# Kernel tuning notes

Measured on AMD Instinct MI355X. Metric: run time of the kernel, lower is better.

The kernel has to match this reference:

```python
import jax, jax.numpy as jnp
import numpy as np

N, E, T = 20000, 320000, 64
INP, EMB, OUT = 128, 16, 3
HEADS, MSIZE, MDIM, KDIM, VDIM = 4, 1024, 128, 64, 64


def setup_inputs() -> dict:
    key = jax.random.key(0)
    ks = iter(jax.random.split(key, 64))

    def nrm(shape, s=0.05):
        return jax.random.normal(next(ks), shape, dtype=jnp.float32) * s

    return dict(
        x=jax.random.normal(next(ks), (N, INP), dtype=jnp.float32),
        edge_index=jax.random.randint(next(ks), (2, E), 0, N),
        index=5,
        inp_types=jax.random.randint(next(ks), (T,), 0, 4),
        log_return=jax.random.normal(next(ks), (T,), dtype=jnp.float32),
        # SAGEConv 1 (SoftmaxAggregation temp t1, lin_l/lin_r, bias=False)
        t1=jnp.ones((1, INP), jnp.float32),
        W1l=nrm((INP, 512)), W1r=nrm((INP, 512)),
        ln1g_w=jnp.ones((512,), jnp.float32), ln1g_b=jnp.zeros((512,), jnp.float32),
        # SAGEConv 2
        t2=jnp.ones((1, 512), jnp.float32),
        W2l=nrm((512, 256)), W2r=nrm((512, 256)),
        ln2g_w=jnp.ones((256,), jnp.float32), ln2g_b=jnp.zeros((256,), jnp.float32),
        # MemPooling(256,128,heads=4,num_clusters=1)
        mp_k=nrm((HEADS, 1, 256), 1.0),
        mp_conv=nrm((HEADS,), 0.5),            # Conv2d(heads,1,1,bias=False)
        mp_lin=nrm((256, 128)),                # Linear(in,out,bias=False)
        fxg_w=nrm((128, 256)), fxg_b=jnp.zeros((256,), jnp.float32),
        # PolicyNet head
        emb=nrm((4, EMB), 1.0),
        fk_w=nrm((256, KDIM)), fk_b=jnp.zeros((KDIM,), jnp.float32),
        fv_w=nrm((256, VDIM)), fv_b=jnp.zeros((VDIM,), jnp.float32),
        # MultiHeadMemory
        mem=nrm((HEADS, MSIZE, MDIM), 1.0),
        mfk_w=nrm((MDIM, KDIM)), mfk_b=jnp.zeros((KDIM,), jnp.float32),
        mfv_w=nrm((MDIM, VDIM)), mfv_b=jnp.zeros((VDIM,), jnp.float32),
        mfx_w=nrm((VDIM * HEADS, VDIM)), mfx_b=jnp.zeros((VDIM,), jnp.float32),
        f1_w=nrm((INP + EMB + 2 * VDIM + 1, 512)),
        n1_w=jnp.ones((512,), jnp.float32), n1_b=jnp.zeros((512,), jnp.float32),
        f2_w=nrm((512, 256)),
        n2_w=jnp.ones((256,), jnp.float32), n2_b=jnp.zeros((256,), jnp.float32),
        f3_w=nrm((256, OUT)), f3_b=jnp.zeros((OUT,), jnp.float32),
    )


def _forward(x, t1, W1l, W1r, ln1g_w, ln1g_b, t2, W2l, W2r, ln2g_w, ln2g_b,
             mp_k, mp_conv, mp_lin, fxg_w, fxg_b, emb, fk_w, fk_b, fv_w, fv_b,
             mem, mfk_w, mfk_b, mfv_w, mfv_b, mfx_w, mfx_b,
             f1_w, n1_w, n1_b, f2_w, n2_w, n2_b, f3_w, f3_b,
             log_return, edge_index, inp_types, index):
    n = x.shape[0]
    src, dst = edge_index[0], edge_index[1]

    def sage(h, t, Wl, Wr):
        hj = h[src]                                    # [E, C] gather
        gate = hj * t                                  # learned softmax temperature
        m = jax.ops.segment_max(gate, dst, num_segments=n)
        e = jnp.exp(gate - m[dst])                     # segment-stable softmax
        s = jax.ops.segment_sum(e, dst, num_segments=n)
        agg = jax.ops.segment_sum(hj * (e / s[dst]), dst, num_segments=n)
        return agg @ Wl + h @ Wr                       # SAGEConv, bias=False

    def graph_ln(h, w, b, eps=1e-5):                   # PyG LayerNorm, mode='graph'
        hc = h - jnp.mean(h)
        return hc / jnp.sqrt(jnp.mean(hc * hc) + eps) * w + b

    h = jax.nn.relu(graph_ln(sage(x, t1, W1l, W1r), ln1g_w, ln1g_b))
    h = jax.nn.relu(graph_ln(sage(h, t2, W2l, W2r), ln2g_w, ln2g_b))

    # MemPooling (single graph => B=1), tau=1: student-t kernel over sq. distances
    H, K, C = mp_k.shape
    kk = mp_k.reshape(H * K, C)
    d2 = jnp.maximum(jnp.sum(kk * kk, 1)[:, None] - 2.0 * (kk @ h.T)
                     + jnp.sum(h * h, 1)[None, :], 0.0)        # [H*K, N]
    dist = 1.0 / (1.0 + d2)
    dist = dist.reshape(H, K, n).transpose(0, 2, 1)[None]      # [1, H, N, K]
    S = dist / jnp.sum(dist, -1, keepdims=True)
    S = jax.nn.softmax(jnp.einsum('h,bhnk->bnk', mp_conv, S), axis=-1)  # [1, N, K]
    zp = jnp.einsum('bnk,nc->bkc', S, h)[:, 0, :]              # squeeze(1), K==1
    z = (zp @ mp_lin) @ fxg_w + fxg_b                          # [1, 256]

    q = jax.nn.softmax(z @ fk_w + fk_b, axis=-1)               # [1, key_dim]
    v = z @ fv_w + fv_b                                        # [1, val_dim]

    # MultiHeadMemory
    km = jax.nn.softmax(mem @ mfk_w + mfk_b, axis=-1)          # [H, M, key]
    vm = mem @ mfv_w + mfv_b                                   # [H, M, val]
    w = jax.nn.softmax(jnp.einsum('bk,hnk->bhn', q, km), axis=-1)
    mv = jnp.einsum('bhn,hnv->bhv', w, vm).reshape(q.shape[0], -1)
    m_out = mv @ mfx_w + mfx_b                                 # [1, val]

    zz = jnp.concatenate([v, m_out], axis=-1)                  # [1, 2*val]
    t_len = inp_types.shape[0]
    xi = jnp.broadcast_to(x[index][None, :], (t_len, x.shape[1]))
    zb = jnp.broadcast_to(zz, (t_len, zz.shape[1]))
    feat = jnp.concatenate([xi, emb[inp_types], log_return.reshape(-1, 1), zb], axis=-1)

    def ln(h2, w2, b2, eps=1e-5):                              # nn.LayerNorm (last dim)
        mu = jnp.mean(h2, -1, keepdims=True)
        hc = h2 - mu
        return hc / jnp.sqrt(jnp.mean(hc * hc, -1, keepdims=True) + eps) * w2 + b2

    h1 = jax.nn.relu(ln(feat @ f1_w, n1_w, n1_b))              # dropout = identity (eval)
    h2 = jax.nn.relu(ln(h1 @ f2_w, n2_w, n2_b))
    return jax.nn.softmax(h2 @ f3_w + f3_b, axis=-1)           # [T, out_dim]


def reference(x, edge_index, index, inp_types, log_return, t1, W1l, W1r, ln1g_w, ln1g_b,
              t2, W2l, W2r, ln2g_w, ln2g_b, mp_k, mp_conv, mp_lin, fxg_w, fxg_b, emb,
              fk_w, fk_b, fv_w, fv_b, mem, mfk_w, mfk_b, mfv_w, mfv_b, mfx_w, mfx_b,
              f1_w, n1_w, n1_b, f2_w, n2_w, n2_b, f3_w, f3_b):
    return _forward(x, t1, W1l, W1r, ln1g_w, ln1g_b, t2, W2l, W2r, ln2g_w, ln2g_b,
                    mp_k, mp_conv, mp_lin, fxg_w, fxg_b, emb, fk_w, fk_b, fv_w, fv_b,
                    mem, mfk_w, mfk_b, mfv_w, mfv_b, mfx_w, mfx_b,
                    f1_w, n1_w, n1_b, f2_w, n2_w, n2_b, f3_w, f3_b,
                    log_return, edge_index, inp_types, index)
```

## Files before the change

### kernel.cpp

```cpp
#include <hip/hip_runtime.h>

typedef __attribute__((ext_vector_type(8))) short bf16x8;
typedef __attribute__((ext_vector_type(8))) unsigned short ushort8_t;
typedef __attribute__((ext_vector_type(4))) float f32x4;

__device__ __forceinline__ unsigned short f2bf(float f) {
    unsigned int x = __float_as_uint(f);
    unsigned int r = x + 0x7fffu + ((x >> 16) & 1u);
    return (unsigned short)(r >> 16);
}
__device__ __forceinline__ float bf2f(unsigned short u) {
    return __uint_as_float(((unsigned int)u) << 16);
}

__global__ void count_kernel(const int* __restrict__ dst, int E, int* __restrict__ counts) {
    int i = blockIdx.x * 256 + threadIdx.x;
    if (i < E) atomicAdd(&counts[dst[i]], 1);
}

template <int CHUNK>
__global__ __launch_bounds__(1024) void scan_kernel(const int* __restrict__ cnt,
                                                    int* __restrict__ off, int n) {
    __shared__ int s[1024];
    int tid = threadIdx.x;
    int base = tid * CHUNK;
    int loc[CHUNK];
    int sum = 0;
#pragma unroll
    for (int i = 0; i < CHUNK; ++i) {
        int idx = base + i;
        int v = (idx < n) ? cnt[idx] : 0;
        sum += v;
        loc[i] = sum;
    }
    s[tid] = sum;
    __syncthreads();
    for (int d = 1; d < 1024; d <<= 1) {
        int t = (tid >= d) ? s[tid - d] : 0;
        __syncthreads();
        s[tid] += t;
        __syncthreads();
    }
    int prev = (tid > 0) ? s[tid - 1] : 0;
    if (tid == 0) off[0] = 0;
#pragma unroll
    for (int i = 0; i < CHUNK; ++i) {
        int idx = base + i;
        if (idx < n) off[idx + 1] = prev + loc[i];
    }
}

__global__ void fill_kernel(const int* __restrict__ src, const int* __restrict__ dst, int E,
                            const int* __restrict__ off, int* __restrict__ cursor,
                            int* __restrict__ srcs) {
    int i = blockIdx.x * 256 + threadIdx.x;
    if (i < E) {
        int d = dst[i];
        int p = atomicAdd(&cursor[d], 1);
        srcs[off[d] + p] = src[i];
    }
}

__global__ __launch_bounds__(256) void cast_bf16(const float* __restrict__ in,
                                                 unsigned short* __restrict__ out, size_t n) {
    size_t stride = (size_t)gridDim.x * 256 * 4;
    for (size_t i = ((size_t)blockIdx.x * 256 + threadIdx.x) * 4; i < n; i += stride) {
        float4 v = *(const float4*)(in + i);
        ushort4 o;
        o.x = f2bf(v.x); o.y = f2bf(v.y); o.z = f2bf(v.z); o.w = f2bf(v.w);
        *(ushort4*)(out + i) = o;
    }
}

__global__ __launch_bounds__(256) void agg512(const unsigned short* __restrict__ h,
                                              const float* __restrict__ t,
                                              const int* __restrict__ off,
                                              const int* __restrict__ srcs,
                                              unsigned short* __restrict__ agg, int n) {
    int wid = threadIdx.x >> 6, lane = threadIdx.x & 63;
    int node = blockIdx.x * 4 + wid;
    if (node >= n) return;
    int beg = off[node], end = off[node + 1];
    int col = lane * 8;
    float tc[8], sE[8], sW[8];
#pragma unroll
    for (int i = 0; i < 8; ++i) { tc[i] = t[col + i]; sE[i] = 0.f; sW[i] = 0.f; }
    int e = beg;
    for (; e + 2 <= end; e += 2) {
        int s0 = srcs[e], s1 = srcs[e + 1];
        ushort8_t u0 = *(const ushort8_t*)(h + (size_t)s0 * 512 + col);
        ushort8_t u1 = *(const ushort8_t*)(h + (size_t)s1 * 512 + col);
#pragma unroll
        for (int i = 0; i < 8; ++i) {
            float v = bf2f(u0[i]);
            float w = __expf(v * tc[i]);
            sE[i] += w; sW[i] += v * w;
        }
#pragma unroll
        for (int i = 0; i < 8; ++i) {
            float v = bf2f(u1[i]);
            float w = __expf(v * tc[i]);
            sE[i] += w; sW[i] += v * w;
        }
    }
    if (e < end) {
        int s0 = srcs[e];
        ushort8_t u0 = *(const ushort8_t*)(h + (size_t)s0 * 512 + col);
#pragma unroll
        for (int i = 0; i < 8; ++i) {
            float v = bf2f(u0[i]);
            float w = __expf(v * tc[i]);
            sE[i] += w; sW[i] += v * w;
        }
    }
    ushort8_t o;
#pragma unroll
    for (int i = 0; i < 8; ++i) o[i] = f2bf((end > beg) ? (sW[i] / sE[i]) : 0.f);
    *(ushort8_t*)(agg + (size_t)node * 512 + col) = o;
}

__global__ __launch_bounds__(256) void agg128(const unsigned short* __restrict__ h,
                                              const float* __restrict__ t,
                                              const int* __restrict__ off,
                                              const int* __restrict__ srcs,
                                              unsigned short* __restrict__ agg, int n) {
    int wid = threadIdx.x >> 6, lane = threadIdx.x & 63;
    int node = blockIdx.x * 4 + wid;
    if (node >= n) return;
    int beg = off[node], end = off[node + 1];
    int col = lane * 2;
    float t0 = t[col], t1 = t[col + 1];
    float e0 = 0.f, e1 = 0.f, w0 = 0.f, w1 = 0.f;
    int e = beg;
    for (; e + 4 <= end; e += 4) {
        int s0 = srcs[e], s1 = srcs[e + 1], s2 = srcs[e + 2], s3 = srcs[e + 3];
        ushort2 u0 = *(const ushort2*)(h + (size_t)s0 * 128 + col);
        ushort2 u1 = *(const ushort2*)(h + (size_t)s1 * 128 + col);
        ushort2 u2 = *(const ushort2*)(h + (size_t)s2 * 128 + col);
        ushort2 u3 = *(const ushort2*)(h + (size_t)s3 * 128 + col);
        {
            float a = bf2f(u0.x), b = bf2f(u0.y);
            float xa = __expf(a * t0), xb = __expf(b * t1);
            e0 += xa; e1 += xb; w0 += a * xa; w1 += b * xb;
        }
        {
            float a = bf2f(u1.x), b = bf2f(u1.y);
            float xa = __expf(a * t0), xb = __expf(b * t1);
            e0 += xa; e1 += xb; w0 += a * xa; w1 += b * xb;
        }
        {
            float a = bf2f(u2.x), b = bf2f(u2.y);
            float xa = __expf(a * t0), xb = __expf(b * t1);
            e0 += xa; e1 += xb; w0 += a * xa; w1 += b * xb;
        }
        {
            float a = bf2f(u3.x), b = bf2f(u3.y);
            float xa = __expf(a * t0), xb = __expf(b * t1);
            e0 += xa; e1 += xb; w0 += a * xa; w1 += b * xb;
        }
    }
    for (; e < end; ++e) {
        int s0 = srcs[e];
        ushort2 u0 = *(const ushort2*)(h + (size_t)s0 * 128 + col);
        float a = bf2f(u0.x), b = bf2f(u0.y);
        float xa = __expf(a * t0), xb = __expf(b * t1);
        e0 += xa; e1 += xb; w0 += a * xa; w1 += b * xb;
    }
    ushort2 o;
    o.x = f2bf((end > beg) ? (w0 / e0) : 0.f);
    o.y = f2bf((end > beg) ? (w1 / e1) : 0.f);
    *(ushort2*)(agg + (size_t)node * 128 + col) = o;
}

__global__ void pack_w(const float* __restrict__ Wl, const float* __restrict__ Wr,
                       int K1, int K2, int N, unsigned short* __restrict__ Bt) {
    int idx = blockIdx.x * 256 + threadIdx.x;
    int Kc = K1 + K2;
    if (idx < N * Kc) {
        int n = idx / Kc;
        int k = idx - n * Kc;
        float v = (k < K1) ? Wl[(size_t)k * N + n] : Wr[(size_t)(k - K1) * N + n];
        Bt[idx] = f2bf(v);
    }
}

__global__ __launch_bounds__(512) void gemm_dual_mfma2(
    const unsigned short* __restrict__ A1, const unsigned short* __restrict__ A2,
    const unsigned short* __restrict__ Bt,
    unsigned short* __restrict__ Cb, double* __restrict__ part,
    int M, int N, int K1, int K2) {
    const int Kc = K1 + K2;
    __shared__ unsigned short As[128 * 40];
    __shared__ unsigned short Bs[256 * 40];
    __shared__ double rs[512], rs2[512];
    int tid = threadIdx.x;
    int lane = tid & 63, w = tid >> 6;
    int wm = w & 1, wn = w >> 1;
    int m0 = blockIdx.y * 128, n0 = blockIdx.x * 256;
    f32x4 acc[4][4] = {};
    int kg = lane >> 4, lr = lane & 15;

    for (int k0 = 0; k0 < Kc; k0 += 32) {
        const unsigned short* Asrc;
        int kk, Ksrc;
        if (k0 < K1) { Asrc = A1; kk = k0; Ksrc = K1; }
        else         { Asrc = A2; kk = k0 - K1; Ksrc = K2; }
        {
            int r = tid >> 2, ch = tid & 3;
            int gr = m0 + r;
            ushort8_t v = {0, 0, 0, 0, 0, 0, 0, 0};
            if (gr < M) v = *(const ushort8_t*)(Asrc + (size_t)gr * Ksrc + kk + ch * 8);
            *(ushort8_t*)&As[r * 40 + ch * 8] = v;
        }
#pragma unroll
        for (int it = 0; it < 2; ++it) {
            int idx = tid + it * 512;
            int r = idx >> 2, ch = idx & 3;
            const unsigned short* srcp = Bt + (size_t)(n0 + r) * Kc + k0 + ch * 8;
            *(ushort8_t*)&Bs[r * 40 + ch * 8] = *(const ushort8_t*)srcp;
        }
        __syncthreads();
        bf16x8 a[4], b[4];
#pragma unroll
        for (int i = 0; i < 4; ++i)
            a[i] = *(bf16x8*)&As[(wm * 64 + i * 16 + lr) * 40 + kg * 8];
#pragma unroll
        for (int j = 0; j < 4; ++j)
            b[j] = *(bf16x8*)&Bs[(wn * 64 + j * 16 + lr) * 40 + kg * 8];
#pragma unroll
        for (int i = 0; i < 4; ++i)
#pragma unroll
            for (int j = 0; j < 4; ++j)
                acc[i][j] = __builtin_amdgcn_mfma_f32_16x16x32_bf16(a[i], b[j], acc[i][j], 0, 0, 0);
        __syncthreads();
    }
    double s = 0, s2 = 0;
#pragma unroll
    for (int i = 0; i < 4; ++i) {
        int rbase = m0 + wm * 64 + i * 16 + kg * 4;
#pragma unroll
        for (int j = 0; j < 4; ++j) {
            int col = n0 + wn * 64 + j * 16 + lr;
#pragma unroll
            for (int reg = 0; reg < 4; ++reg) {
                int row = rbase + reg;
                if (row < M) {
                    float v = acc[i][j][reg];
                    Cb[(size_t)row * N + col] = f2bf(v);
                    s += v;
                    s2 += (double)v * v;
                }
            }
        }
    }
    rs[tid] = s;
    rs2[tid] = s2;
    __syncthreads();
    for (int d = 256; d; d >>= 1) {
        if (tid < d) { rs[tid] += rs[tid + d]; rs2[tid] += rs2[tid + d]; }
        __syncthreads();
    }
    if (tid == 0) {
        int bid = blockIdx.y * gridDim.x + blockIdx.x;
        part[bid * 2] = rs[0];
        part[bid * 2 + 1] = rs2[0];
    }
}

__global__ __launch_bounds__(256) void red_stats2d(const double* __restrict__ part, int nb,
                                                   float invn, float* __restrict__ stats) {
    __shared__ double rs[256], rs2[256];
    int tid = threadIdx.x;
    double s = 0, s2 = 0;
    for (int b = tid; b < nb; b += 256) { s += part[b * 2]; s2 += part[b * 2 + 1]; }
    rs[tid] = s; rs2[tid] = s2;
    __syncthreads();
    for (int d = 128; d; d >>= 1) {
        if (tid < d) { rs[tid] += rs[tid + d]; rs2[tid] += rs2[tid + d]; }
        __syncthreads();
    }
    if (tid == 0) {
        float mu = (float)(rs[0] * invn);
        float var = (float)(rs2[0] * invn) - mu * mu;
        stats[0] = mu;
        stats[1] = rsqrtf(var + 1e-5f);
    }
}

template <int C>
__global__ __launch_bounds__(256) void ln_relu_ip(unsigned short* __restrict__ z,
                                                  const float* __restrict__ w,
                                                  const float* __restrict__ b,
                                                  const float* __restrict__ stats, size_t n) {
    float mu = stats[0], inv = stats[1];
    size_t stride = (size_t)gridDim.x * 256 * 4;
    for (size_t i = ((size_t)blockIdx.x * 256 + threadIdx.x) * 4; i < n; i += stride) {
        ushort4 v = *(const ushort4*)(z + i);
        int c = (int)(i & (C - 1));
        ushort4 o;
        o.x = f2bf(fmaxf((bf2f(v.x) - mu) * inv * w[c] + b[c], 0.f));
        o.y = f2bf(fmaxf((bf2f(v.y) - mu) * inv * w[c + 1] + b[c + 1], 0.f));
        o.z = f2bf(fmaxf((bf2f(v.z) - mu) * inv * w[c + 2] + b[c + 2], 0.f));
        o.w = f2bf(fmaxf((bf2f(v.w) - mu) * inv * w[c + 3] + b[c + 3], 0.f));
        *(ushort4*)(z + i) = o;
    }
}

__global__ __launch_bounds__(256) void colsum_t(const unsigned short* __restrict__ h2,
                                                float* __restrict__ cspartT, int n) {
    __shared__ float red[8 * 256];
    int tid = threadIdx.x;
    int cg = tid & 31;
    int rl = tid >> 5;
    int rows_per = (n + gridDim.x - 1) / gridDim.x;
    int r0 = blockIdx.x * rows_per;
    int r1 = min(n, r0 + rows_per);
    int c8 = cg * 8;
    float acc[8] = {};
    for (int r = r0 + rl; r < r1; r += 8) {
        ushort8_t u = *(const ushort8_t*)(h2 + (size_t)r * 256 + c8);
#pragma unroll
        for (int i = 0; i < 8; ++i) acc[i] += bf2f(u[i]);
    }
#pragma unroll
    for (int i = 0; i < 8; ++i) red[rl * 256 + c8 + i] = acc[i];
    __syncthreads();
    float s = 0;
#pragma unroll
    for (int r = 0; r < 8; ++r) s += red[r * 256 + tid];
    cspartT[tid * 64 + blockIdx.x] = s;
}

__global__ __launch_bounds__(256) void zqv_kernel(const float* __restrict__ cspartT,
                                                  const float* __restrict__ mp_lin,
                                                  const float* __restrict__ fxg_w,
                                                  const float* __restrict__ fxg_b,
                                                  const float* __restrict__ fk_w,
                                                  const float* __restrict__ fk_b,
                                                  const float* __restrict__ fv_w,
                                                  const float* __restrict__ fv_b,
                                                  float* __restrict__ qv) {
    __shared__ float zp_s[256], u_s[128], z_s[256], ql_s[64];
    __shared__ float part_s[1024];
    int tid = threadIdx.x;
    {
        float s = 0;
        const float* p = cspartT + tid * 64;
#pragma unroll
        for (int i = 0; i < 16; ++i) {
            float4 v = *(const float4*)(p + i * 4);
            s += v.x + v.y + v.z + v.w;
        }
        zp_s[tid] = s;
    }
    __syncthreads();
    {
        int og = tid & 31, kc = tid >> 5;
        int j4 = og * 4;
        f32x4 a = {0.f, 0.f, 0.f, 0.f};
        for (int ci = 0; ci < 32; ++ci) {
            int c = kc * 32 + ci;
            float4 w = *(const float4*)(mp_lin + (size_t)c * 128 + j4);
            float zc = zp_s[c];
            a[0] += zc * w.x; a[1] += zc * w.y; a[2] += zc * w.z; a[3] += zc * w.w;
        }
#pragma unroll
        for (int i = 0; i < 4; ++i) part_s[kc * 128 + j4 + i] = a[i];
    }
    __syncthreads();
    if (tid < 128) {
        float s = 0;
#pragma unroll
        for (int kc = 0; kc < 8; ++kc) s += part_s[kc * 128 + tid];
        u_s[tid] = s;
    }
    __syncthreads();
    {
        int og = tid & 63, kc = tid >> 6;
        int j4 = og * 4;
        f32x4 a = {0.f, 0.f, 0.f, 0.f};
        for (int ci = 0; ci < 32; ++ci) {
            int c = kc * 32 + ci;
            float4 w = *(const float4*)(fxg_w + (size_t)c * 256 + j4);
            float uc = u_s[c];
            a[0] += uc * w.x; a[1] += uc * w.y; a[2] += uc * w.z; a[3] += uc * w.w;
        }
#pragma unroll
        for (int i = 0; i < 4; ++i) part_s[kc * 256 + j4 + i] = a[i];
    }
    __syncthreads();
    {
        float s = fxg_b[tid];
#pragma unroll
        for (int kc = 0; kc < 4; ++kc) s += part_s[kc * 256 + tid];
        z_s[tid] = s;
    }
    __syncthreads();
    {
        int og = tid & 15, kc = tid >> 4;
        int j4 = og * 4;
        f32x4 a = {0.f, 0.f, 0.f, 0.f};
        for (int ci = 0; ci < 16; ++ci) {
            int c = kc * 16 + ci;
            float4 w = *(const float4*)(fk_w + (size_t)c * 64 + j4);
            float zc = z_s[c];
            a[0] += zc * w.x; a[1] += zc * w.y; a[2] += zc * w.z; a[3] += zc * w.w;
        }
#pragma unroll
        for (int i = 0; i < 4; ++i) part_s[kc * 64 + j4 + i] = a[i];
    }
    __syncthreads();
    if (tid < 64) {
        float s = fk_b[tid];
#pragma unroll
        for (int kc = 0; kc < 16; ++kc) s += part_s[kc * 64 + tid];
        ql_s[tid] = s;
    }
    __syncthreads();
    {
        int og = tid & 15, kc = tid >> 4;
        int j4 = og * 4;
        f32x4 a = {0.f, 0.f, 0.f, 0.f};
        for (int ci = 0; ci < 16; ++ci) {
            int c = kc * 16 + ci;
            float4 w = *(const float4*)(fv_w + (size_t)c * 64 + j4);
            float zc = z_s[c];
            a[0] += zc * w.x; a[1] += zc * w.y; a[2] += zc * w.z; a[3] += zc * w.w;
        }
#pragma unroll
        for (int i = 0; i < 4; ++i) part_s[kc * 64 + j4 + i] = a[i];
    }
    __syncthreads();
    if (tid < 64) {
        float mx = ql_s[tid];
        for (int d = 32; d; d >>= 1) mx = fmaxf(mx, __shfl_xor(mx, d));
        float e = __expf(ql_s[tid] - mx);
        float s = e;
        for (int d = 32; d; d >>= 1) s += __shfl_xor(s, d);
        qv[tid] = e / s;
        float vv = fv_b[tid];
#pragma unroll
        for (int kc = 0; kc < 16; ++kc) vv += part_s[kc * 64 + tid];
        qv[64 + tid] = vv;
    }
}

__global__ __launch_bounds__(256) void mem_kv_logit(const float* __restrict__ mem,
                                                    const float* __restrict__ mfk_w,
                                                    const float* __restrict__ mfk_b,
                                                    const float* __restrict__ mfv_w,
                                                    const float* __restrict__ mfv_b,
                                                    const float* __restrict__ qv,
                                                    float* __restrict__ logits,
                                                    float* __restrict__ vm) {
    __shared__ float rows[4][128];
    __shared__ float qs[64];
    int tid = threadIdx.x;
    int r0 = blockIdx.x * 4;
    if (tid < 64) qs[tid] = qv[tid];
    for (int i = tid; i < 512; i += 256) rows[i >> 7][i & 127] = mem[(size_t)r0 * 128 + i];
    __syncthreads();
    int lr = tid >> 6;
    int lane = tid & 63;
    const float* row = rows[lr];
    float kl = mfk_b[lane], vl = mfv_b[lane];
#pragma unroll 8
    for (int c = 0; c < 128; ++c) {
        float rv = row[c];
        kl += rv * mfk_w[c * 64 + lane];
        vl += rv * mfv_w[c * 64 + lane];
    }
    float mx = kl;
    for (int d = 32; d; d >>= 1) mx = fmaxf(mx, __shfl_xor(mx, d));
    float e = __expf(kl - mx);
    float s = e;
    for (int d = 32; d; d >>= 1) s += __shfl_xor(s, d);
    float kval = e / s;
    float wl = kval * qs[lane];
    for (int d = 32; d; d >>= 1) wl += __shfl_xor(wl, d);
    size_t gr = (size_t)(r0 + lr);
    if (lane == 0) logits[gr] = wl;
    vm[gr * 64 + lane] = vl;
}

__global__ __launch_bounds__(256) void attend_part(const float* __restrict__ logits,
                                                   const float* __restrict__ vm,
                                                   float* __restrict__ part) {
    int b = blockIdx.x;
    int h = b >> 4;
    int s0 = (b & 15) * 64;
    int tid = threadIdx.x;
    __shared__ float els[64];
    __shared__ float pr[4][64];
    __shared__ float lmax_s, lsum_s;
    if (tid < 64) {
        float lg = logits[h * 1024 + s0 + tid];
        float m = lg;
        for (int d = 32; d; d >>= 1) m = fmaxf(m, __shfl_xor(m, d));
        float e = __expf(lg - m);
        els[tid] = e;
        float s = e;
        for (int d = 32; d; d >>= 1) s += __shfl_xor(s, d);
        if (tid == 0) { lmax_s = m; lsum_s = s; }
    }
    __syncthreads();
    int dd = tid & 63, g = tid >> 6;
    float acc = 0;
    for (int s = g; s < 64; s += 4)
        acc += els[s] * vm[((size_t)h * 1024 + s0 + s) * 64 + dd];
    pr[g][dd] = acc;
    __syncthreads();
    if (tid < 64) {
        float pv = pr[0][tid] + pr[1][tid] + pr[2][tid] + pr[3][tid];
        part[b * 66 + 2 + tid] = pv;
        if (tid == 0) { part[b * 66] = lmax_s; part[b * 66 + 1] = lsum_s; }
    }
}

__global__ __launch_bounds__(256) void attend_final(const float* __restrict__ part,
                                                    const float* __restrict__ mfx_w,
                                                    const float* __restrict__ mfx_b,
                                                    float* __restrict__ m_out) {
    __shared__ float mv[256];
    __shared__ float part_s[1024];
    int tid = threadIdx.x;
    int h = tid >> 6, dd = tid & 63;
    float gmax = -1e30f;
#pragma unroll
    for (int p = 0; p < 16; ++p) gmax = fmaxf(gmax, part[(h * 16 + p) * 66]);
    float total = 0.f, acc = 0.f;
#pragma unroll
    for (int p = 0; p < 16; ++p) {
        float sc = __expf(part[(h * 16 + p) * 66] - gmax);
        total += part[(h * 16 + p) * 66 + 1] * sc;
        acc += part[(h * 16 + p) * 66 + 2 + dd] * sc;
    }
    mv[h * 64 + dd] = acc / total;
    __syncthreads();
    {
        int og = tid & 15, kc = tid >> 4;
        int j4 = og * 4;
        f32x4 a = {0.f, 0.f, 0.f, 0.f};
        for (int ci = 0; ci < 16; ++ci) {
            int c = kc * 16 + ci;
            float4 w = *(const float4*)(mfx_w + (size_t)c * 64 + j4);
            float mc = mv[c];
            a[0] += mc * w.x; a[1] += mc * w.y; a[2] += mc * w.z; a[3] += mc * w.w;
        }
#pragma unroll
        for (int i = 0; i < 4; ++i) part_s[kc * 64 + j4 + i] = a[i];
    }
    __syncthreads();
    if (tid < 64) {
        float s = mfx_b[tid];
#pragma unroll
        for (int kc = 0; kc < 16; ++kc) s += part_s[kc * 64 + tid];
        m_out[tid] = s;
    }
}

__device__ __forceinline__ float block_sum_256(float v, float* red) {
    int tid = threadIdx.x;
    red[tid] = v;
    __syncthreads();
    for (int d = 128; d; d >>= 1) { if (tid < d) red[tid] += red[tid + d]; __syncthreads(); }
    float r = red[0];
    __syncthreads();
    return r;
}

__global__ __launch_bounds__(256) void head_kernel(
    const float* __restrict__ x, const int* __restrict__ index_p,
    const int* __restrict__ inp_types, const float* __restrict__ log_return,
    const float* __restrict__ emb, const float* __restrict__ qv,
    const float* __restrict__ m_out, const float* __restrict__ f1_w,
    const float* __restrict__ n1_w, const float* __restrict__ n1_b,
    const float* __restrict__ f2_w, const float* __restrict__ n2_w,
    const float* __restrict__ n2_b, const float* __restrict__ f3_w,
    const float* __restrict__ f3_b, float* __restrict__ out) {
    __shared__ float feat[273];
    __shared__ float h1[512];
    __shared__ float h2[256];
    __shared__ float red[256];
    __shared__ float l3[3];
    int r = blockIdx.x, tid = threadIdx.x;
    int idx = index_p[0];
    for (int i = tid; i < 273; i += 256) {
        float val;
        if (i < 128) val = x[(size_t)idx * 128 + i];
        else if (i < 144) val = emb[inp_types[r] * 16 + (i - 128)];
        else if (i == 144) val = log_return[r];
        else if (i < 209) val = qv[64 + (i - 145)];
        else val = m_out[i - 209];
        feat[i] = val;
    }
    __syncthreads();
    float a0 = 0, a1 = 0;
    for (int c = 0; c < 273; ++c) {
        float f = feat[c];
        a0 += f * f1_w[c * 512 + tid];
        a1 += f * f1_w[c * 512 + tid + 256];
    }
    float mu = block_sum_256(a0 + a1, red) / 512.f;
    float c0 = a0 - mu, c1 = a1 - mu;
    float var = block_sum_256(c0 * c0 + c1 * c1, red) / 512.f;
    float inv = rsqrtf(var + 1e-5f);
    h1[tid] = fmaxf(c0 * inv * n1_w[tid] + n1_b[tid], 0.f);
    h1[tid + 256] = fmaxf(c1 * inv * n1_w[tid + 256] + n1_b[tid + 256], 0.f);
    __syncthreads();
    float b0 = 0;
    for (int c = 0; c < 512; ++c) b0 += h1[c] * f2_w[c * 256 + tid];
    float mu2 = block_sum_256(b0, red) / 256.f;
    float cc = b0 - mu2;
    float var2 = block_sum_256(cc * cc, red) / 256.f;
    float inv2 = rsqrtf(var2 + 1e-5f);
    h2[tid] = fmaxf(cc * inv2 * n2_w[tid] + n2_b[tid], 0.f);
    __syncthreads();
    if (tid < 3) {
        float a = f3_b[tid];
        for (int c = 0; c < 256; ++c) a += h2[c] * f3_w[c * 3 + tid];
        l3[tid] = a;
    }
    __syncthreads();
    if (tid < 3) {
        float mx = fmaxf(l3[0], fmaxf(l3[1], l3[2]));
        float s = __expf(l3[0] - mx) + __expf(l3[1] - mx) + __expf(l3[2] - mx);
        out[r * 3 + tid] = __expf(l3[tid] - mx) / s;
    }
}

extern "C" void kernel_launch(void* const* d_in, const int* in_sizes, int n_in,
                              void* d_out, int out_size, void* d_ws, size_t ws_size,
                              hipStream_t stream) {
    const float* x = (const float*)d_in[0];
    const int* ei = (const int*)d_in[1];
    const int* index_p = (const int*)d_in[2];
    const int* inp_types = (const int*)d_in[3];
    const float* log_return = (const float*)d_in[4];
    const float* t1 = (const float*)d_in[5];
    const float* W1l = (const float*)d_in[6];
    const float* W1r = (const float*)d_in[7];
    const float* ln1g_w = (const float*)d_in[8];
    const float* ln1g_b = (const float*)d_in[9];
    const float* t2 = (const float*)d_in[10];
    const float* W2l = (const float*)d_in[11];
    const float* W2r = (const float*)d_in[12];
    const float* ln2g_w = (const float*)d_in[13];
    const float* ln2g_b = (const float*)d_in[14];
    const float* mp_lin = (const float*)d_in[17];
    const float* fxg_w = (const float*)d_in[18];
    const float* fxg_b = (const float*)d_in[19];
    const float* emb = (const float*)d_in[20];
    const float* fk_w = (const float*)d_in[21];
    const float* fk_b = (const float*)d_in[22];
    const float* fv_w = (const float*)d_in[23];
    const float* fv_b = (const float*)d_in[24];
    const float* mem = (const float*)d_in[25];
    const float* mfk_w = (const float*)d_in[26];
    const float* mfk_b = (const float*)d_in[27];
    const float* mfv_w = (const float*)d_in[28];
    const float* mfv_b = (const float*)d_in[29];
    const float* mfx_w = (const float*)d_in[30];
    const float* mfx_b = (const float*)d_in[31];
    const float* f1_w = (const float*)d_in[32];
    const float* n1_w = (const float*)d_in[33];
    const float* n1_b = (const float*)d_in[34];
    const float* f2_w = (const float*)d_in[35];
    const float* n2_w = (const float*)d_in[36];
    const float* n2_b = (const float*)d_in[37];
    const float* f3_w = (const float*)d_in[38];
    const float* f3_b = (const float*)d_in[39];
    float* out = (float*)d_out;

    int n = in_sizes[0] / 128;
    int E = in_sizes[1] / 2;
    int T = in_sizes[3];
    const int* src = ei;
    const int* dst = ei + E;

    char* w = (char*)d_ws;
    auto alloc = [&](size_t bytes) {
        char* p = w;
        w += (bytes + 255) & ~(size_t)255;
        return p;
    };
    int* counts = (int*)alloc((size_t)n * 4);
    int* off = (int*)alloc((size_t)(n + 1) * 4);
    int* srcs = (int*)alloc((size_t)E * 4);
    unsigned short* xb = (unsigned short*)alloc((size_t)n * 128 * 2);
    unsigned short* agg1b = (unsigned short*)alloc((size_t)n * 128 * 2);
    unsigned short* z1b = (unsigned short*)alloc((size_t)n * 512 * 2);
    unsigned short* agg2b = (unsigned short*)alloc((size_t)n * 512 * 2);
    unsigned short* z2b = (unsigned short*)alloc((size_t)n * 256 * 2);
    double* partd = (double*)alloc(1024 * 2 * 8);
    float* stats = (float*)alloc(2 * 4);
    float* cspartT = (float*)alloc(256 * 64 * 4);
    float* qv = (float*)alloc(128 * 4);
    float* logits = (float*)alloc((size_t)4 * 1024 * 4);
    float* vm = (float*)alloc((size_t)4 * 1024 * 64 * 4);
    float* apart = (float*)alloc(64 * 66 * 4);
    float* m_out = (float*)alloc(64 * 4);
    unsigned short* Bt1 = (unsigned short*)alloc((size_t)512 * 256 * 2);
    unsigned short* Bt2 = (unsigned short*)alloc((size_t)256 * 1024 * 2);

    int nblk_e = (E + 255) / 256;
    int mblk = (n + 127) / 128;

    hipMemsetAsync(counts, 0, (size_t)n * 4, stream);
    count_kernel<<<nblk_e, 256, 0, stream>>>(dst, E, counts);
    scan_kernel<20><<<1, 1024, 0, stream>>>(counts, off, n);
    hipMemsetAsync(counts, 0, (size_t)n * 4, stream);
    fill_kernel<<<nblk_e, 256, 0, stream>>>(src, dst, E, off, counts, srcs);

    pack_w<<<(512 * 256 + 255) / 256, 256, 0, stream>>>(W1l, W1r, 128, 128, 512, Bt1);
    pack_w<<<(256 * 1024 + 255) / 256, 256, 0, stream>>>(W2l, W2r, 512, 512, 256, Bt2);
    cast_bf16<<<1024, 256, 0, stream>>>(x, xb, (size_t)n * 128);

    agg128<<<(n + 3) / 4, 256, 0, stream>>>(xb, t1, off, srcs, agg1b, n);
    gemm_dual_mfma2<<<dim3(2, mblk), 512, 0, stream>>>(agg1b, xb, Bt1, z1b, partd, n, 512, 128, 128);
    red_stats2d<<<1, 256, 0, stream>>>(partd, 2 * mblk, 1.0f / ((float)n * 512.f), stats);
    ln_relu_ip<512><<<1024, 256, 0, stream>>>(z1b, ln1g_w, ln1g_b, stats, (size_t)n * 512);

    agg512<<<(n + 3) / 4, 256, 0, stream>>>(z1b, t2, off, srcs, agg2b, n);
    gemm_dual_mfma2<<<dim3(1, mblk), 512, 0, stream>>>(agg2b, z1b, Bt2, z2b, partd, n, 256, 512, 512);
    red_stats2d<<<1, 256, 0, stream>>>(partd, mblk, 1.0f / ((float)n * 256.f), stats);
    ln_relu_ip<256><<<512, 256, 0, stream>>>(z2b, ln2g_w, ln2g_b, stats, (size_t)n * 256);

    colsum_t<<<64, 256, 0, stream>>>(z2b, cspartT, n);
    zqv_kernel<<<1, 256, 0, stream>>>(cspartT, mp_lin, fxg_w, fxg_b, fk_w, fk_b, fv_w, fv_b, qv);

    mem_kv_logit<<<1024, 256, 0, stream>>>(mem, mfk_w, mfk_b, mfv_w, mfv_b, qv, logits, vm);
    attend_part<<<64, 256, 0, stream>>>(logits, vm, apart);
    attend_final<<<1, 256, 0, stream>>>(apart, mfx_w, mfx_b, m_out);

    head_kernel<<<T, 256, 0, stream>>>(x, index_p, inp_types, log_return, emb, qv, m_out,
                                       f1_w, n1_w, n1_b, f2_w, n2_w, n2_b, f3_w, f3_b, out);
}
```

Baseline: 292.2 us.

## Use direct global-to-LDS loads in GEMM, fuse LN stats, deepen aggregation unroll

The GEMM tile loads now use global_load_lds to copy straight into unpadded LDS, skipping the register round trip. The separate stats-reduction kernels are folded into the LayerNorm kernels, and the scan kernel zeroes the counts so one memset goes away. The aggregation loops are unrolled further, with exp2f on pre-scaled temperatures. The unpadded LDS layout may cause bank conflicts, and the A-tile load drops the row bounds check, so the last partial tile can read past M (an extra padding allocation is added).

```diff
diff --git a/kernel.cpp b/kernel.cpp
--- a/kernel.cpp
+++ b/kernel.cpp
@@ -12,6 +12,12 @@
 __device__ __forceinline__ float bf2f(unsigned short u) {
     return __uint_as_float(((unsigned int)u) << 16);
 }
+__device__ __forceinline__ void load_lds16(const void* g, void* l) {
+    __builtin_amdgcn_global_load_lds((const __attribute__((address_space(1))) void*)g,
+                                     (__attribute__((address_space(3))) void*)l, 16, 0, 0);
+}
+
+#define LOG2E 1.44269504089f
 
 __global__ void count_kernel(const int* __restrict__ dst, int E, int* __restrict__ counts) {
     int i = blockIdx.x * 256 + threadIdx.x;
@@ -19,7 +25,7 @@
 }
 
 template <int CHUNK>
-__global__ __launch_bounds__(1024) void scan_kernel(const int* __restrict__ cnt,
+__global__ __launch_bounds__(1024) void scan_kernel(int* __restrict__ cnt,
                                                     int* __restrict__ off, int n) {
     __shared__ int s[1024];
     int tid = threadIdx.x;
@@ -29,7 +35,8 @@
 #pragma unroll
     for (int i = 0; i < CHUNK; ++i) {
         int idx = base + i;
-        int v = (idx < n) ? cnt[idx] : 0;
+        int v = 0;
+        if (idx < n) { v = cnt[idx]; cnt[idx] = 0; }
         sum += v;
         loc[i] = sum;
     }
@@ -84,35 +91,28 @@
     int col = lane * 8;
     float tc[8], sE[8], sW[8];
 #pragma unroll
-    for (int i = 0; i < 8; ++i) { tc[i] = t[col + i]; sE[i] = 0.f; sW[i] = 0.f; }
+    for (int i = 0; i < 8; ++i) { tc[i] = t[col + i] * LOG2E; sE[i] = 0.f; sW[i] = 0.f; }
+#define P8(u)                                      \
+    _Pragma("unroll") for (int i = 0; i < 8; ++i) { \
+        float v = bf2f(u[i]);                       \
+        float wv = exp2f(v * tc[i]);                \
+        sE[i] += wv; sW[i] += v * wv;               \
+    }
     int e = beg;
-    for (; e + 2 <= end; e += 2) {
-        int s0 = srcs[e], s1 = srcs[e + 1];
+    for (; e + 4 <= end; e += 4) {
+        int s0 = srcs[e], s1 = srcs[e + 1], s2 = srcs[e + 2], s3 = srcs[e + 3];
         ushort8_t u0 = *(const ushort8_t*)(h + (size_t)s0 * 512 + col);
         ushort8_t u1 = *(const ushort8_t*)(h + (size_t)s1 * 512 + col);
-#pragma unroll
-        for (int i = 0; i < 8; ++i) {
-            float v = bf2f(u0[i]);
-            float w = __expf(v * tc[i]);
-            sE[i] += w; sW[i] += v * w;
-        }
-#pragma unroll
-        for (int i = 0; i < 8; ++i) {
-            float v = bf2f(u1[i]);
-            float w = __expf(v * tc[i]);
-            sE[i] += w; sW[i] += v * w;
-        }
-    }
-    if (e < end) {
+        ushort8_t u2 = *(const ushort8_t*)(h + (size_t)s2 * 512 + col);
+        ushort8_t u3 = *(const ushort8_t*)(h + (size_t)s3 * 512 + col);
+        P8(u0) P8(u1) P8(u2) P8(u3)
+    }
+    for (; e < end; ++e) {
         int s0 = srcs[e];
         ushort8_t u0 = *(const ushort8_t*)(h + (size_t)s0 * 512 + col);
-#pragma unroll
-        for (int i = 0; i < 8; ++i) {
-            float v = bf2f(u0[i]);
-            float w = __expf(v * tc[i]);
-            sE[i] += w; sW[i] += v * w;
-        }
-    }
+        P8(u0)
+    }
+#undef P8
     ushort8_t o;
 #pragma unroll
     for (int i = 0; i < 8; ++i) o[i] = f2bf((end > beg) ? (sW[i] / sE[i]) : 0.f);
@@ -129,43 +129,31 @@
     if (node >= n) return;
     int beg = off[node], end = off[node + 1];
     int col = lane * 2;
-    float t0 = t[col], t1 = t[col + 1];
+    float t0 = t[col] * LOG2E, t1 = t[col + 1] * LOG2E;
     float e0 = 0.f, e1 = 0.f, w0 = 0.f, w1 = 0.f;
+#define P2(u)                                          \
+    {                                                  \
+        float a = bf2f(u.x), b = bf2f(u.y);            \
+        float xa = exp2f(a * t0), xb = exp2f(b * t1);  \
+        e0 += xa; e1 += xb; w0 += a * xa; w1 += b * xb; \
+    }
     int e = beg;
-    for (; e + 4 <= end; e += 4) {
-        int s0 = srcs[e], s1 = srcs[e + 1], s2 = srcs[e + 2], s3 = srcs[e + 3];
-        ushort2 u0 = *(const ushort2*)(h + (size_t)s0 * 128 + col);
-        ushort2 u1 = *(const ushort2*)(h + (size_t)s1 * 128 + col);
-        ushort2 u2 = *(const ushort2*)(h + (size_t)s2 * 128 + col);
-        ushort2 u3 = *(const ushort2*)(h + (size_t)s3 * 128 + col);
-        {
-            float a = bf2f(u0.x), b = bf2f(u0.y);
-            float xa = __expf(a * t0), xb = __expf(b * t1);
-            e0 += xa; e1 += xb; w0 += a * xa; w1 += b * xb;
-        }
-        {
-            float a = bf2f(u1.x), b = bf2f(u1.y);
-            float xa = __expf(a * t0), xb = __expf(b * t1);
-            e0 += xa; e1 += xb; w0 += a * xa; w1 += b * xb;
-        }
-        {
-            float a = bf2f(u2.x), b = bf2f(u2.y);
-            float xa = __expf(a * t0), xb = __expf(b * t1);
-            e0 += xa; e1 += xb; w0 += a * xa; w1 += b * xb;
-        }
-        {
-            float a = bf2f(u3.x), b = bf2f(u3.y);
-            float xa = __expf(a * t0), xb = __expf(b * t1);
-            e0 += xa; e1 += xb; w0 += a * xa; w1 += b * xb;
-        }
+    for (; e + 8 <= end; e += 8) {
+        ushort2 u0 = *(const ushort2*)(h + (size_t)srcs[e] * 128 + col);
+        ushort2 u1 = *(const ushort2*)(h + (size_t)srcs[e + 1] * 128 + col);
+        ushort2 u2 = *(const ushort2*)(h + (size_t)srcs[e + 2] * 128 + col);
+        ushort2 u3 = *(const ushort2*)(h + (size_t)srcs[e + 3] * 128 + col);
+        ushort2 u4 = *(const ushort2*)(h + (size_t)srcs[e + 4] * 128 + col);
+        ushort2 u5 = *(const ushort2*)(h + (size_t)srcs[e + 5] * 128 + col);
+        ushort2 u6 = *(const ushort2*)(h + (size_t)srcs[e + 6] * 128 + col);
+        ushort2 u7 = *(const ushort2*)(h + (size_t)srcs[e + 7] * 128 + col);
+        P2(u0) P2(u1) P2(u2) P2(u3) P2(u4) P2(u5) P2(u6) P2(u7)
     }
     for (; e < end; ++e) {
-        int s0 = srcs[e];
-        ushort2 u0 = *(const ushort2*)(h + (size_t)s0 * 128 + col);
-        float a = bf2f(u0.x), b = bf2f(u0.y);
-        float xa = __expf(a * t0), xb = __expf(b * t1);
-        e0 += xa; e1 += xb; w0 += a * xa; w1 += b * xb;
-    }
+        ushort2 u0 = *(const ushort2*)(h + (size_t)srcs[e] * 128 + col);
+        P2(u0)
+    }
+#undef P2
     ushort2 o;
     o.x = f2bf((end > beg) ? (w0 / e0) : 0.f);
     o.y = f2bf((end > beg) ? (w1 / e1) : 0.f);
@@ -190,8 +178,8 @@
     unsigned short* __restrict__ Cb, double* __restrict__ part,
     int M, int N, int K1, int K2) {
     const int Kc = K1 + K2;
-    __shared__ unsigned short As[128 * 40];
-    __shared__ unsigned short Bs[256 * 40];
+    __shared__ unsigned short As[128 * 32];
+    __shared__ unsigned short Bs[256 * 32];
     __shared__ double rs[512], rs2[512];
     int tid = threadIdx.x;
     int lane = tid & 63, w = tid >> 6;
@@ -199,34 +187,25 @@
     int m0 = blockIdx.y * 128, n0 = blockIdx.x * 256;
     f32x4 acc[4][4] = {};
     int kg = lane >> 4, lr = lane & 15;
+    int ar = tid >> 2, ach = tid & 3;
+    int br0 = tid >> 2, bch = tid & 3;
 
     for (int k0 = 0; k0 < Kc; k0 += 32) {
         const unsigned short* Asrc;
         int kk, Ksrc;
         if (k0 < K1) { Asrc = A1; kk = k0; Ksrc = K1; }
         else         { Asrc = A2; kk = k0 - K1; Ksrc = K2; }
-        {
-            int r = tid >> 2, ch = tid & 3;
-            int gr = m0 + r;
-            ushort8_t v = {0, 0, 0, 0, 0, 0, 0, 0};
-            if (gr < M) v = *(const ushort8_t*)(Asrc + (size_t)gr * Ksrc + kk + ch * 8);
-            *(ushort8_t*)&As[r * 40 + ch * 8] = v;
-        }
-#pragma unroll
-        for (int it = 0; it < 2; ++it) {
-            int idx = tid + it * 512;
-            int r = idx >> 2, ch = idx & 3;
-            const unsigned short* srcp = Bt + (size_t)(n0 + r) * Kc + k0 + ch * 8;
-            *(ushort8_t*)&Bs[r * 40 + ch * 8] = *(const ushort8_t*)srcp;
-        }
+        load_lds16(Asrc + (size_t)(m0 + ar) * Ksrc + kk + ach * 8, &As[tid * 8]);
+        load_lds16(Bt + (size_t)(n0 + br0) * Kc + k0 + bch * 8, &Bs[tid * 8]);
+        load_lds16(Bt + (size_t)(n0 + 128 + br0) * Kc + k0 + bch * 8, &Bs[(tid + 512) * 8]);
         __syncthreads();
         bf16x8 a[4], b[4];
 #pragma unroll
         for (int i = 0; i < 4; ++i)
-            a[i] = *(bf16x8*)&As[(wm * 64 + i * 16 + lr) * 40 + kg * 8];
+            a[i] = *(bf16x8*)&As[(wm * 64 + i * 16 + lr) * 32 + kg * 8];
 #pragma unroll
         for (int j = 0; j < 4; ++j)
-            b[j] = *(bf16x8*)&Bs[(wn * 64 + j * 16 + lr) * 40 + kg * 8];
+            b[j] = *(bf16x8*)&Bs[(wn * 64 + j * 16 + lr) * 32 + kg * 8];
 #pragma unroll
         for (int i = 0; i < 4; ++i)
 #pragma unroll
@@ -267,32 +246,26 @@
     }
 }
 
-__global__ __launch_bounds__(256) void red_stats2d(const double* __restrict__ part, int nb,
-                                                   float invn, float* __restrict__ stats) {
-    __shared__ double rs[256], rs2[256];
-    int tid = threadIdx.x;
-    double s = 0, s2 = 0;
-    for (int b = tid; b < nb; b += 256) { s += part[b * 2]; s2 += part[b * 2 + 1]; }
-    rs[tid] = s; rs2[tid] = s2;
-    __syncthreads();
-    for (int d = 128; d; d >>= 1) {
-        if (tid < d) { rs[tid] += rs[tid + d]; rs2[tid] += rs2[tid + d]; }
-        __syncthreads();
-    }
-    if (tid == 0) {
-        float mu = (float)(rs[0] * invn);
-        float var = (float)(rs2[0] * invn) - mu * mu;
-        stats[0] = mu;
-        stats[1] = rsqrtf(var + 1e-5f);
-    }
-}
-
 template <int C>
 __global__ __launch_bounds__(256) void ln_relu_ip(unsigned short* __restrict__ z,
                                                   const float* __restrict__ w,
                                                   const float* __restrict__ b,
-                                                  const float* __restrict__ stats, size_t n) {
-    float mu = stats[0], inv = stats[1];
+                                                  const double* __restrict__ part, int nb,
+                                                  float invn, size_t n) {
+    __shared__ float st[2];
+    if (threadIdx.x < 64) {
+        double s = 0, s2 = 0;
+        for (int i = threadIdx.x; i < nb; i += 64) { s += part[2 * i]; s2 += part[2 * i + 1]; }
+        for (int d = 32; d; d >>= 1) { s += __shfl_down(s, d); s2 += __shfl_down(s2, d); }
+        if (threadIdx.x == 0) {
+            float mu = (float)(s * invn);
+            float var = (float)(s2 * invn) - mu * mu;
+            st[0] = mu;
+            st[1] = rsqrtf(var + 1e-5f);
+        }
+    }
+    __syncthreads();
+    float mu = st[0], inv = st[1];
     size_t stride = (size_t)gridDim.x * 256 * 4;
     for (size_t i = ((size_t)blockIdx.x * 256 + threadIdx.x) * 4; i < n; i += stride) {
         ushort4 v = *(const ushort4*)(z + i);
@@ -693,7 +666,6 @@
     unsigned short* agg2b = (unsigned short*)alloc((size_t)n * 512 * 2);
     unsigned short* z2b = (unsigned short*)alloc((size_t)n * 256 * 2);
     double* partd = (double*)alloc(1024 * 2 * 8);
-    float* stats = (float*)alloc(2 * 4);
     float* cspartT = (float*)alloc(256 * 64 * 4);
     float* qv = (float*)alloc(128 * 4);
     float* logits = (float*)alloc((size_t)4 * 1024 * 4);
@@ -702,6 +674,7 @@
     float* m_out = (float*)alloc(64 * 4);
     unsigned short* Bt1 = (unsigned short*)alloc((size_t)512 * 256 * 2);
     unsigned short* Bt2 = (unsigned short*)alloc((size_t)256 * 1024 * 2);
+    alloc(4096);
 
     int nblk_e = (E + 255) / 256;
     int mblk = (n + 127) / 128;
@@ -709,7 +682,6 @@
     hipMemsetAsync(counts, 0, (size_t)n * 4, stream);
     count_kernel<<<nblk_e, 256, 0, stream>>>(dst, E, counts);
     scan_kernel<20><<<1, 1024, 0, stream>>>(counts, off, n);
-    hipMemsetAsync(counts, 0, (size_t)n * 4, stream);
     fill_kernel<<<nblk_e, 256, 0, stream>>>(src, dst, E, off, counts, srcs);
 
     pack_w<<<(512 * 256 + 255) / 256, 256, 0, stream>>>(W1l, W1r, 128, 128, 512, Bt1);
@@ -718,13 +690,13 @@
 
     agg128<<<(n + 3) / 4, 256, 0, stream>>>(xb, t1, off, srcs, agg1b, n);
     gemm_dual_mfma2<<<dim3(2, mblk), 512, 0, stream>>>(agg1b, xb, Bt1, z1b, partd, n, 512, 128, 128);
-    red_stats2d<<<1, 256, 0, stream>>>(partd, 2 * mblk, 1.0f / ((float)n * 512.f), stats);
-    ln_relu_ip<512><<<1024, 256, 0, stream>>>(z1b, ln1g_w, ln1g_b, stats, (size_t)n * 512);
+    ln_relu_ip<512><<<1024, 256, 0, stream>>>(z1b, ln1g_w, ln1g_b, partd, 2 * mblk,
+                                              1.0f / ((float)n * 512.f), (size_t)n * 512);
 
     agg512<<<(n + 3) / 4, 256, 0, stream>>>(z1b, t2, off, srcs, agg2b, n);
     gemm_dual_mfma2<<<dim3(1, mblk), 512, 0, stream>>>(agg2b, z1b, Bt2, z2b, partd, n, 256, 512, 512);
-    red_stats2d<<<1, 256, 0, stream>>>(partd, mblk, 1.0f / ((float)n * 256.f), stats);
-    ln_relu_ip<256><<<512, 256, 0, stream>>>(z2b, ln2g_w, ln2g_b, stats, (size_t)n * 256);
+    ln_relu_ip<256><<<512, 256, 0, stream>>>(z2b, ln2g_w, ln2g_b, partd, mblk,
+                                             1.0f / ((float)n * 256.f), (size_t)n * 256);
 
     colsum_t<<<64, 256, 0, stream>>>(z2b, cspartT, n);
     zqv_kernel<<<1, 256, 0, stream>>>(cspartT, mp_lin, fxg_w, fxg_b, fk_w, fk_b, fv_w, fv_b, qv);
```

Result: slower. 318.1 us (+8.9%).
